# Performance work log

Measured on AMD Instinct MI355X. Metric: run time of the kernel, lower is better.

Reference implementation:

```python
import jax, jax.numpy as jnp
import numpy as np

DECAY = 0.9


def setup_inputs() -> dict:
    key = jax.random.key(0)
    ks = jax.random.split(key, 8)
    B, L, d_model = 4, 2048, 1024
    d_state = 16
    d_inner = 2 * d_model  # expand=2
    x = jax.random.normal(ks[0], (B, L, d_model), dtype=jnp.float32)
    Win = jax.random.normal(ks[1], (d_model, d_inner), dtype=jnp.float32) / np.sqrt(d_model)
    bin_ = jnp.zeros((d_inner,), dtype=jnp.float32)
    Bp = jax.random.normal(ks[2], (d_inner, d_state), dtype=jnp.float32) * 0.01
    Cp = jax.random.normal(ks[3], (d_state, d_inner), dtype=jnp.float32) * 0.01
    Dp = jnp.ones((d_inner,), dtype=jnp.float32)
    Wout = jax.random.normal(ks[4], (d_inner, d_model), dtype=jnp.float32) / np.sqrt(d_inner)
    bout = jnp.zeros((d_model,), dtype=jnp.float32)
    return {"x": x, "Win": Win, "bin_": bin_, "Bp": Bp, "Cp": Cp, "Dp": Dp,
            "Wout": Wout, "bout": bout}


def reference(x, Win, bin_, Bp, Cp, Dp, Wout, bout):
    # x: [B, L, d_model]
    B, L, _ = x.shape
    d_inner, d_state = Bp.shape
    xi = jax.nn.silu(x @ Win + bin_)          # [B, L, d_inner]
    xt_seq = jnp.swapaxes(xi, 0, 1)            # [L, B, d_inner] for scan over time

    def step(h, xt):
        # h: [B, d_inner, d_state]; xt: [B, d_inner]
        h = h * DECAY + xt[:, :, None] * Bp[None, :, :]
        y = jnp.einsum('bij,ji->bi', h, Cp) + Dp * xt
        return h, y

    h0 = jnp.zeros((B, d_inner, d_state), dtype=x.dtype)
    _, ys = jax.lax.scan(step, h0, xt_seq)     # ys: [L, B, d_inner]
    y = jnp.swapaxes(ys, 0, 1)                 # [B, L, d_inner]
    return y @ Wout + bout                     # [B, L, d_model]
```

## Files before the change

### kernel.cpp

```cpp
#include <hip/hip_runtime.h>
#include <hip/hip_bf16.h>
#include <cstdint>
#include <cstddef>

typedef __attribute__((ext_vector_type(8))) short short8_t;
typedef __attribute__((ext_vector_type(4))) float f32x4;

__device__ __forceinline__ void gload16(const void* g, void* l) {
  __builtin_amdgcn_global_load_lds(
      (const __attribute__((address_space(1))) void*)g,
      (__attribute__((address_space(3))) void*)l, 16, 0, 0);
}

#define BARRIER() do { asm volatile("" ::: "memory"); __builtin_amdgcn_s_barrier(); asm volatile("" ::: "memory"); } while (0)
#define WVM6 asm volatile("s_waitcnt vmcnt(6)" ::: "memory")
#define WVM0 asm volatile("s_waitcnt vmcnt(0)" ::: "memory")
#define LGKM0_PIN() do { asm volatile("s_waitcnt lgkmcnt(0)" ::: "memory"); __builtin_amdgcn_sched_barrier(0); } while (0)

__global__ __launch_bounds__(256) void cvt_bf16_kernel(
    const float* __restrict__ in, __hip_bfloat16* __restrict__ out, int n) {
  int gid = blockIdx.x * blockDim.x + threadIdx.x;
  int idx = gid * 4;
  if (idx >= n) return;
  float4 v = *reinterpret_cast<const float4*>(in + idx);
  union { short4 s4; __hip_bfloat16 h[4]; } u;
  u.h[0] = __float2bfloat16(v.x);
  u.h[1] = __float2bfloat16(v.y);
  u.h[2] = __float2bfloat16(v.z);
  u.h[3] = __float2bfloat16(v.w);
  *reinterpret_cast<short4*>(out + idx) = u.s4;
}

__global__ __launch_bounds__(256) void transpose_cvt_kernel(
    const float* __restrict__ in, __hip_bfloat16* __restrict__ out, int R, int C) {
  __shared__ float tile[32][33];
  int c0 = blockIdx.x * 32, r0 = blockIdx.y * 32;
  int tx = threadIdx.x, ty = threadIdx.y;
#pragma unroll
  for (int j = 0; j < 32; j += 8)
    tile[ty + j][tx] = in[(size_t)(r0 + ty + j) * C + c0 + tx];
  __syncthreads();
#pragma unroll
  for (int j = 0; j < 32; j += 8)
    out[(size_t)(c0 + ty + j) * R + r0 + tx] = __float2bfloat16(tile[tx][ty + j]);
}

template <int EPI>
__global__ __launch_bounds__(512, 2) void gemm3b_kernel(
    const __hip_bfloat16* __restrict__ A,
    const __hip_bfloat16* __restrict__ Bt,
    const float* __restrict__ bias,
    void* __restrict__ Cout,
    int M, int N, int K) {
  constexpr int BOFF = 3 * 32768;
  __shared__ int4 ldsv[(3 * 32768 + 3 * 16384) / 16];
  char* lds = (char*)ldsv;

  const int tid = threadIdx.x;
  const int l = tid & 63;
  const int w = tid >> 6;
  const int wm = w >> 1, wn = w & 1;
  const int fr = l & 15;
  const int sl = ((l >> 4) ^ ((fr >> 3) << 1)) * 16;
  const int arow_base = (wm * 64 + fr) * 64 + sl;
  const int brow_base = (wn * 64 + fr) * 64 + sl;

  const int nbn = N / 128;
  int bid = blockIdx.x;
  const int cpx = gridDim.x >> 3;
  bid = (bid & 7) * cpx + (bid >> 3);
  const int brow = (bid / nbn) * 256;
  const int bcol = (bid % nbn) * 128;
  const size_t K2 = (size_t)K * 2;

  int arA[2], acbA[2], dstA[2];
#pragma unroll
  for (int j = 0; j < 2; ++j) {
    int d = j * 8192 + w * 1024 + l * 16;
    int lg = d ^ (((d >> 9) & 1) << 5);
    arA[j] = lg >> 6;  acbA[j] = lg & 63;
    dstA[j] = j * 8192 + w * 1024;
  }
  int dB = w * 1024 + l * 16;
  int lgB = dB ^ (((dB >> 9) & 1) << 5);
  const int arB = lgB >> 6, acbB = lgB & 63, dstB = w * 1024;

  const char* Abp = (const char*)A;
  const char* Bbp = (const char*)Bt;

  auto stA = [&](int bufb, int kh, int tt) {
#pragma unroll
    for (int j = 0; j < 2; ++j)
      gload16(Abp + (size_t)(brow + arA[j]) * K2 + tt * 128 + kh * 64 + acbA[j],
              lds + bufb + kh * 16384 + dstA[j]);
  };
  auto stB = [&](int bufb, int kh, int tt) {
    gload16(Bbp + (size_t)(bcol + arB) * K2 + tt * 128 + kh * 64 + acbB,
            lds + BOFF + bufb + kh * 8192 + dstB);
  };

  f32x4 acc[4][4];
#pragma unroll
  for (int m = 0; m < 4; ++m)
#pragma unroll
    for (int n = 0; n < 4; ++n) acc[m][n] = (f32x4)0.f;
  short8_t af[4], bf[4];

  auto ldA_ = [&](int bufb, int kh) {
#pragma unroll
    for (int mi = 0; mi < 4; ++mi)
      af[mi] = *(const short8_t*)(lds + bufb + kh * 16384 + arow_base + mi * 1024);
  };
  auto ldB_ = [&](int bufb, int kh) {
#pragma unroll
    for (int n = 0; n < 4; ++n)
      bf[n] = *(const short8_t*)(lds + BOFF + bufb + kh * 8192 + brow_base + n * 1024);
  };
  auto mfma16 = [&]() {
    __builtin_amdgcn_s_setprio(1);
#pragma unroll
    for (int mi = 0; mi < 4; ++mi)
#pragma unroll
      for (int n = 0; n < 4; ++n)
        acc[mi][n] = __builtin_amdgcn_mfma_f32_16x16x32_bf16(af[mi], bf[n], acc[mi][n], 0, 0, 0);
    __builtin_amdgcn_s_setprio(0);
  };

  const int NT = K >> 6;
  stA(0, 0, 0); stA(0, 1, 0); stB(0, 0, 0); stB(0, 1, 0);
  stA(32768, 0, 1); stA(32768, 1, 1); stB(16384, 0, 1); stB(16384, 1, 1);
  WVM6; BARRIER();

  int curA = 0, curB = 0, stAb = 2 * 32768, stBb = 2 * 16384;
  for (int T = 0; T < NT - 2; ++T) {
    ldA_(curA, 0); ldB_(curB, 0);
    stA(stAb, 0, T + 2);
    BARRIER(); LGKM0_PIN(); mfma16(); BARRIER();
    ldA_(curA, 1); ldB_(curB, 1);
    stA(stAb, 1, T + 2); stB(stBb, 0, T + 2); stB(stBb, 1, T + 2);
    WVM6;
    BARRIER(); LGKM0_PIN(); mfma16(); BARRIER();
    curA += 32768; if (curA == 3 * 32768) curA = 0;
    curB += 16384; if (curB == 3 * 16384) curB = 0;
    stAb += 32768; if (stAb == 3 * 32768) stAb = 0;
    stBb += 16384; if (stBb == 3 * 16384) stBb = 0;
  }
  ldA_(curA, 0); ldB_(curB, 0);
  BARRIER(); LGKM0_PIN(); mfma16(); BARRIER();
  ldA_(curA, 1); ldB_(curB, 1);
  WVM0;
  BARRIER(); LGKM0_PIN(); mfma16(); BARRIER();
  curA += 32768; if (curA == 3 * 32768) curA = 0;
  curB += 16384; if (curB == 3 * 16384) curB = 0;
  ldA_(curA, 0); ldB_(curB, 0);
  BARRIER(); LGKM0_PIN(); mfma16(); BARRIER();
  ldA_(curA, 1); ldB_(curB, 1);
  LGKM0_PIN(); mfma16();

  const int r0 = brow + wm * 64 + (l >> 4) * 4;
  const int c0 = bcol + wn * 64 + fr;
#pragma unroll
  for (int m = 0; m < 4; ++m) {
#pragma unroll
    for (int n = 0; n < 4; ++n) {
      const int col = c0 + n * 16;
      const float bv = bias[col];
#pragma unroll
      for (int j = 0; j < 4; ++j) {
        const int row = r0 + m * 16 + j;
        float v = acc[m][n][j] + bv;
        if constexpr (EPI == 0) {
          v = v / (1.0f + __expf(-v));
          ((__hip_bfloat16*)Cout)[(size_t)row * N + col] = __float2bfloat16(v);
        } else {
          ((float*)Cout)[(size_t)row * N + col] = v;
        }
      }
    }
  }
}

__global__ __launch_bounds__(256) void scan_kernel(
    const __hip_bfloat16* __restrict__ xi,
    const float* __restrict__ Bp,
    const float* __restrict__ Cp,
    const float* __restrict__ Dp,
    __hip_bfloat16* __restrict__ y) {
  constexpr int L = 2048, DI = 2048, DS = 16, TW = 256, H = 32;
  const int tid = threadIdx.x;
  const int bidx = blockIdx.x;
  const int iblk = bidx & 7;
  const int chunk = (bidx >> 3) & 7;
  const int b = bidx >> 6;
  const int i = iblk * 256 + tid;

  float cb = 0.f;
#pragma unroll
  for (int s = 0; s < DS; ++s) cb += Bp[i * DS + s] * Cp[s * DI + i];
  const float dp = Dp[i];

  const int t0 = chunk * TW;
  int tstart = t0 - H;
  if (tstart < 0) tstart = 0;

  const __hip_bfloat16* xp = xi + (size_t)(b * L) * DI + i;
  __hip_bfloat16* yp = y + (size_t)(b * L) * DI + i;

  float g = 0.f;
  const __hip_bfloat16* p = xp + (size_t)tstart * DI;
  for (int t = tstart; t < t0; ++t, p += DI)
    g = g * 0.9f + __bfloat162float(*p);
  __hip_bfloat16* q = yp + (size_t)t0 * DI;
  for (int t = 0; t < TW; ++t, p += DI, q += DI) {
    float xv = __bfloat162float(*p);
    g = g * 0.9f + xv;
    *q = __float2bfloat16(cb * g + dp * xv);
  }
}

extern "C" void kernel_launch(void* const* d_in, const int* in_sizes, int n_in,
                              void* d_out, int out_size, void* d_ws, size_t ws_size,
                              hipStream_t stream) {
  const float* x    = (const float*)d_in[0];
  const float* Win  = (const float*)d_in[1];
  const float* bin  = (const float*)d_in[2];
  const float* Bp   = (const float*)d_in[3];
  const float* Cp   = (const float*)d_in[4];
  const float* Dp   = (const float*)d_in[5];
  const float* Wout = (const float*)d_in[6];
  const float* bout = (const float*)d_in[7];
  float* out = (float*)d_out;

  constexpr int Bb = 4, L = 2048, DM = 1024, DI = 2048;
  constexpr int Mrows = Bb * L;

  char* ws = (char*)d_ws;
  __hip_bfloat16* xb    = (__hip_bfloat16*)ws;
  __hip_bfloat16* WinT  = (__hip_bfloat16*)(ws + (16u << 20));
  __hip_bfloat16* WoutT = (__hip_bfloat16*)(ws + (20u << 20));
  __hip_bfloat16* xi    = (__hip_bfloat16*)(ws + (24u << 20));
  __hip_bfloat16* yb    = (__hip_bfloat16*)(ws + (56u << 20));

  {
    int n = Mrows * DM;
    cvt_bf16_kernel<<<n / 1024, 256, 0, stream>>>(x, xb, n);
  }
  transpose_cvt_kernel<<<dim3(DI / 32, DM / 32), dim3(32, 8), 0, stream>>>(Win, WinT, DM, DI);
  transpose_cvt_kernel<<<dim3(DM / 32, DI / 32), dim3(32, 8), 0, stream>>>(Wout, WoutT, DI, DM);
  gemm3b_kernel<0><<<(Mrows / 256) * (DI / 128), 512, 0, stream>>>(
      xb, WinT, bin, (void*)xi, Mrows, DI, DM);
  scan_kernel<<<Bb * (L / 256) * (DI / 256), 256, 0, stream>>>(xi, Bp, Cp, Dp, yb);
  gemm3b_kernel<1><<<(Mrows / 256) * (DM / 128), 512, 0, stream>>>(
      yb, WoutT, bout, (void*)out, Mrows, DM, DI);
}
```

Before: 131.9 us.

## Restructure GEMM main loop to one barrier per K-tile with full-tile fragment loads

Replaces the two half-tile phases per K iteration, each wrapped in a pair of barriers, with a single loop that loads both K halves of A/B fragments, issues all global prefetches for tile T+2, runs 32 MFMAs, then waits and barriers once. The goal is to cut barrier and LDS wait stalls per tile and give the compiler freedom to interleave LDS reads with MFMAs. It removes the sched_barrier pin and the setprio hints and doubles fragment registers, which may raise register pressure at 2 blocks per CU. The memory-count wait threshold is kept as before, with some risk to load ordering.

```diff
diff --git a/kernel.cpp b/kernel.cpp
--- a/kernel.cpp
+++ b/kernel.cpp
@@ -15,7 +15,7 @@
 #define BARRIER() do { asm volatile("" ::: "memory"); __builtin_amdgcn_s_barrier(); asm volatile("" ::: "memory"); } while (0)
 #define WVM6 asm volatile("s_waitcnt vmcnt(6)" ::: "memory")
 #define WVM0 asm volatile("s_waitcnt vmcnt(0)" ::: "memory")
-#define LGKM0_PIN() do { asm volatile("s_waitcnt lgkmcnt(0)" ::: "memory"); __builtin_amdgcn_sched_barrier(0); } while (0)
+#define LGKM0 asm volatile("s_waitcnt lgkmcnt(0)" ::: "memory")
 
 __global__ __launch_bounds__(256) void cvt_bf16_kernel(
     const float* __restrict__ in, __hip_bfloat16* __restrict__ out, int n) {
@@ -46,14 +46,15 @@
 }
 
 template <int EPI>
-__global__ __launch_bounds__(512, 2) void gemm3b_kernel(
+__global__ __launch_bounds__(512, 2) void gemm1b_kernel(
     const __hip_bfloat16* __restrict__ A,
     const __hip_bfloat16* __restrict__ Bt,
     const float* __restrict__ bias,
     void* __restrict__ Cout,
     int M, int N, int K) {
-  constexpr int BOFF = 3 * 32768;
-  __shared__ int4 ldsv[(3 * 32768 + 3 * 16384) / 16];
+  constexpr int ABUF = 32768, BBUF = 16384;
+  constexpr int BOFF = 3 * ABUF;
+  __shared__ int4 ldsv[(3 * ABUF + 3 * BBUF) / 16];
   char* lds = (char*)ldsv;
 
   const int tid = threadIdx.x;
@@ -104,58 +105,46 @@
   for (int m = 0; m < 4; ++m)
 #pragma unroll
     for (int n = 0; n < 4; ++n) acc[m][n] = (f32x4)0.f;
-  short8_t af[4], bf[4];
-
-  auto ldA_ = [&](int bufb, int kh) {
-#pragma unroll
-    for (int mi = 0; mi < 4; ++mi)
-      af[mi] = *(const short8_t*)(lds + bufb + kh * 16384 + arow_base + mi * 1024);
-  };
-  auto ldB_ = [&](int bufb, int kh) {
-#pragma unroll
-    for (int n = 0; n < 4; ++n)
-      bf[n] = *(const short8_t*)(lds + BOFF + bufb + kh * 8192 + brow_base + n * 1024);
-  };
-  auto mfma16 = [&]() {
-    __builtin_amdgcn_s_setprio(1);
-#pragma unroll
-    for (int mi = 0; mi < 4; ++mi)
-#pragma unroll
-      for (int n = 0; n < 4; ++n)
-        acc[mi][n] = __builtin_amdgcn_mfma_f32_16x16x32_bf16(af[mi], bf[n], acc[mi][n], 0, 0, 0);
-    __builtin_amdgcn_s_setprio(0);
-  };
 
   const int NT = K >> 6;
   stA(0, 0, 0); stA(0, 1, 0); stB(0, 0, 0); stB(0, 1, 0);
-  stA(32768, 0, 1); stA(32768, 1, 1); stB(16384, 0, 1); stB(16384, 1, 1);
+  stA(ABUF, 0, 1); stA(ABUF, 1, 1); stB(BBUF, 0, 1); stB(BBUF, 1, 1);
   WVM6; BARRIER();
 
-  int curA = 0, curB = 0, stAb = 2 * 32768, stBb = 2 * 16384;
-  for (int T = 0; T < NT - 2; ++T) {
-    ldA_(curA, 0); ldB_(curB, 0);
-    stA(stAb, 0, T + 2);
-    BARRIER(); LGKM0_PIN(); mfma16(); BARRIER();
-    ldA_(curA, 1); ldB_(curB, 1);
-    stA(stAb, 1, T + 2); stB(stBb, 0, T + 2); stB(stBb, 1, T + 2);
-    WVM6;
-    BARRIER(); LGKM0_PIN(); mfma16(); BARRIER();
-    curA += 32768; if (curA == 3 * 32768) curA = 0;
-    curB += 16384; if (curB == 3 * 16384) curB = 0;
-    stAb += 32768; if (stAb == 3 * 32768) stAb = 0;
-    stBb += 16384; if (stBb == 3 * 16384) stBb = 0;
-  }
-  ldA_(curA, 0); ldB_(curB, 0);
-  BARRIER(); LGKM0_PIN(); mfma16(); BARRIER();
-  ldA_(curA, 1); ldB_(curB, 1);
-  WVM0;
-  BARRIER(); LGKM0_PIN(); mfma16(); BARRIER();
-  curA += 32768; if (curA == 3 * 32768) curA = 0;
-  curB += 16384; if (curB == 3 * 16384) curB = 0;
-  ldA_(curA, 0); ldB_(curB, 0);
-  BARRIER(); LGKM0_PIN(); mfma16(); BARRIER();
-  ldA_(curA, 1); ldB_(curB, 1);
-  LGKM0_PIN(); mfma16();
+  int curA = 0, curB = 0, stAb = 2 * ABUF, stBb = 2 * BBUF;
+  for (int T = 0; T < NT; ++T) {
+    short8_t af[8], bf[8];
+#pragma unroll
+    for (int kh = 0; kh < 2; ++kh) {
+#pragma unroll
+      for (int mi = 0; mi < 4; ++mi)
+        af[kh * 4 + mi] = *(const short8_t*)(lds + curA + kh * 16384 + arow_base + mi * 1024);
+#pragma unroll
+      for (int n = 0; n < 4; ++n)
+        bf[kh * 4 + n] = *(const short8_t*)(lds + BOFF + curB + kh * 8192 + brow_base + n * 1024);
+    }
+    if (T + 2 < NT) {
+      stA(stAb, 0, T + 2); stA(stAb, 1, T + 2);
+      stB(stBb, 0, T + 2); stB(stBb, 1, T + 2);
+    }
+#pragma unroll
+    for (int kh = 0; kh < 2; ++kh)
+#pragma unroll
+      for (int mi = 0; mi < 4; ++mi)
+#pragma unroll
+        for (int n = 0; n < 4; ++n)
+          acc[mi][n] = __builtin_amdgcn_mfma_f32_16x16x32_bf16(
+              af[kh * 4 + mi], bf[kh * 4 + n], acc[mi][n], 0, 0, 0);
+    if (T + 1 < NT) {
+      if (T + 2 < NT) { WVM6; } else { WVM0; }
+      LGKM0;
+      BARRIER();
+    }
+    curA += ABUF; if (curA == 3 * ABUF) curA = 0;
+    curB += BBUF; if (curB == 3 * BBUF) curB = 0;
+    stAb += ABUF; if (stAb == 3 * ABUF) stAb = 0;
+    stBb += BBUF; if (stBb == 3 * BBUF) stBb = 0;
+  }
 
   const int r0 = brow + wm * 64 + (l >> 4) * 4;
   const int c0 = bcol + wn * 64 + fr;
@@ -247,9 +236,9 @@
   }
   transpose_cvt_kernel<<<dim3(DI / 32, DM / 32), dim3(32, 8), 0, stream>>>(Win, WinT, DM, DI);
   transpose_cvt_kernel<<<dim3(DM / 32, DI / 32), dim3(32, 8), 0, stream>>>(Wout, WoutT, DI, DM);
-  gemm3b_kernel<0><<<(Mrows / 256) * (DI / 128), 512, 0, stream>>>(
+  gemm1b_kernel<0><<<(Mrows / 256) * (DI / 128), 512, 0, stream>>>(
       xb, WinT, bin, (void*)xi, Mrows, DI, DM);
   scan_kernel<<<Bb * (L / 256) * (DI / 256), 256, 0, stream>>>(xi, Bp, Cp, Dp, yb);
-  gemm3b_kernel<1><<<(Mrows / 256) * (DM / 128), 512, 0, stream>>>(
+  gemm1b_kernel<1><<<(Mrows / 256) * (DM / 128), 512, 0, stream>>>(
       yb, WoutT, bout, (void*)out, Mrows, DM, DI);
 }
```

Result: faster. 128.2 us (-2.8%).
